# Optimization experiments

Measured on AMD Instinct MI355X. Metric: run time of the kernel, lower is better.

## Reference

```python
import jax, jax.numpy as jnp
import numpy as np

K = 32
TEMPERATURE = 0.1
RTOL, ATOL = 1e-5, 1e-5


def _embed(x, W1, b1, W2, b2, W3, b3):
    h = jax.nn.gelu(x @ W1.T + b1, approximate=False)
    h = jax.nn.gelu(h @ W2.T + b2, approximate=False)
    return jax.nn.sigmoid(h @ W3.T + b3)


def setup_inputs() -> dict:
    key = jax.random.key(0)
    ks = jax.random.split(key, 9)
    Q, N, D_IN, D_E = 256, 16384, 256, 64
    s = lambda fan_in: 1.0 / np.sqrt(fan_in)
    return {
        "x": jax.random.normal(ks[0], (Q, D_IN), jnp.float32),
        "support_x": jax.random.normal(ks[1], (N, D_IN), jnp.float32),
        "support_labels": jax.random.uniform(ks[2], (N, 1), jnp.float32),
        "W1": jax.random.normal(ks[3], (D_E, D_IN), jnp.float32) * s(D_IN),
        "b1": jax.random.normal(ks[4], (D_E,), jnp.float32) * s(D_IN),
        "W2": jax.random.normal(ks[5], (D_E, D_E), jnp.float32) * s(D_E),
        "b2": jax.random.normal(ks[6], (D_E,), jnp.float32) * s(D_E),
        "W3": jax.random.normal(ks[7], (D_E, D_E), jnp.float32) * s(D_E),
        "b3": jax.random.normal(ks[8], (D_E,), jnp.float32) * s(D_E),
    }


def reference(x, support_x, support_labels, W1, b1, W2, b2, W3, b3):
    # query embeddings [Q, D]; support embeddings [N, D] (set_support is no_grad)
    q = _embed(x, W1, b1, W2, b2, W3, b3)
    s = jax.lax.stop_gradient(_embed(support_x, W1, b1, W2, b2, W3, b3))
    # torch.cdist p=2 via expanded squared distances
    d2 = (jnp.sum(q * q, -1)[:, None] + jnp.sum(s * s, -1)[None, :]
          - 2.0 * (q @ s.T))
    dist = jnp.sqrt(jnp.maximum(d2, 0.0))  # [Q, N]
    # isclose mask: |q - s| <= atol + rtol*|s|, all over feature dim
    close = jnp.abs(q[:, None, :] - s[None, :, :]) <= (ATOL + RTOL * jnp.abs(s)[None, :, :])
    mask = jnp.all(close, axis=-1)  # [Q, N]
    dist = jnp.where(mask, jnp.inf, dist)
    # top-k smallest distances
    neg_top, idx = jax.lax.top_k(-dist, K)  # [Q, K]
    topd = -neg_top
    neighbor_labels = support_labels[idx].squeeze(-1)  # [Q, K]
    weights = jax.nn.softmax(-topd / TEMPERATURE, axis=1)
    return jnp.sum(weights * neighbor_labels, axis=1)  # [Q]
```

## Files before the change

kernel.cpp:

```cpp
#include <hip/hip_runtime.h>
#include <math.h>

#define D_IN   256
#define D_E    64
#define N_SUP  16384
#define NQ     256
#define KSEL   32
#define RTOLC  1e-5f
#define ATOLC  1e-5f
#define INV_T  10.0f

#define CHUNK  1024
#define NCH    16
#define QG     8
#define NQG    32

typedef unsigned long long ull;

__device__ __forceinline__ float gelu_exact(float x) {
    return 0.5f * x * (1.0f + erff(x * 0.70710678118654752440f));
}

__global__ __launch_bounds__(256) void prep_w(
    const float* __restrict__ W1, const float* __restrict__ W2,
    const float* __restrict__ W3,
    float* __restrict__ W1T, float* __restrict__ W2T, float* __restrict__ W3T)
{
    const int t = blockIdx.x * 256 + threadIdx.x;
    const int stride = gridDim.x * 256;
    for (int o = t; o < D_E * D_IN; o += stride) {
        int f = o >> 8, k = o & 255;
        W1T[k * D_E + f] = W1[o];
    }
    for (int o = t; o < D_E * D_E; o += stride) {
        int f = o >> 6, k = o & 63;
        W2T[k * D_E + f] = W2[o];
        W3T[k * D_E + f] = W3[o];
    }
}

__global__ __launch_bounds__(512, 6) void embed_kernel(
    const float* __restrict__ sx, const float* __restrict__ x,
    const float* __restrict__ W1T, const float* __restrict__ b1,
    const float* __restrict__ W2T, const float* __restrict__ b2,
    const float* __restrict__ W3T, const float* __restrict__ b3,
    float* __restrict__ s_emb, float* __restrict__ s_norm,
    float* __restrict__ q_emb, float* __restrict__ q_norm)
{
    __shared__ float xc[64][65];
    __shared__ float hA[64][65];
    __shared__ float hB[64][65];
    __shared__ float nsum[64][9];

    const int tid  = threadIdx.x;
    const int lane = tid & 63;
    const int wv   = tid >> 6;
    const int f0   = __builtin_amdgcn_readfirstlane(wv * 8);
    const bool isq = blockIdx.x >= (N_SUP / 64);
    const float* src = isq ? (x + (size_t)(blockIdx.x - N_SUP / 64) * 64 * D_IN)
                           : (sx + (size_t)blockIdx.x * 64 * D_IN);

    float acc[8];
    #pragma unroll
    for (int i = 0; i < 8; ++i) acc[i] = b1[f0 + i];

    for (int kc = 0; kc < 4; ++kc) {
        __syncthreads();
        #pragma unroll
        for (int i = 0; i < 2; ++i) {
            int g   = i * 512 + tid;
            int row = g >> 4;
            int c4  = g & 15;
            float4 v = *reinterpret_cast<const float4*>(
                src + (size_t)row * D_IN + kc * 64 + c4 * 4);
            xc[c4 * 4 + 0][row] = v.x; xc[c4 * 4 + 1][row] = v.y;
            xc[c4 * 4 + 2][row] = v.z; xc[c4 * 4 + 3][row] = v.w;
        }
        __syncthreads();
        const float* wbase = W1T + (size_t)(kc * 64) * D_E + f0;
        #pragma unroll 8
        for (int k = 0; k < 64; ++k) {
            float xk = xc[k][lane];
            const float* wk = wbase + k * D_E;
            #pragma unroll
            for (int f = 0; f < 8; ++f) acc[f] = fmaf(wk[f], xk, acc[f]);
        }
    }
    #pragma unroll
    for (int i = 0; i < 8; ++i) hA[f0 + i][lane] = gelu_exact(acc[i]);
    __syncthreads();

    float a2[8];
    #pragma unroll
    for (int i = 0; i < 8; ++i) a2[i] = b2[f0 + i];
    #pragma unroll 8
    for (int k = 0; k < D_E; ++k) {
        float hk = hA[k][lane];
        const float* wk = W2T + k * D_E + f0;
        #pragma unroll
        for (int f = 0; f < 8; ++f) a2[f] = fmaf(wk[f], hk, a2[f]);
    }
    #pragma unroll
    for (int i = 0; i < 8; ++i) hB[f0 + i][lane] = gelu_exact(a2[i]);
    __syncthreads();

    float a3[8];
    #pragma unroll
    for (int i = 0; i < 8; ++i) a3[i] = b3[f0 + i];
    #pragma unroll 8
    for (int k = 0; k < D_E; ++k) {
        float hk = hB[k][lane];
        const float* wk = W3T + k * D_E + f0;
        #pragma unroll
        for (int f = 0; f < 8; ++f) a3[f] = fmaf(wk[f], hk, a3[f]);
    }
    float e[8];
    float np = 0.0f;
    #pragma unroll
    for (int i = 0; i < 8; ++i) {
        e[i] = 1.0f / (1.0f + expf(-a3[i]));
        np = fmaf(e[i], e[i], np);
    }

    const int rowl = isq ? (blockIdx.x - N_SUP / 64) * 64 + lane
                         : blockIdx.x * 64 + lane;
    float* E   = isq ? q_emb  : s_emb;
    float* Nrm = isq ? q_norm : s_norm;
    float* erow = E + (size_t)rowl * D_E + f0;
    *reinterpret_cast<float4*>(erow)     = make_float4(e[0], e[1], e[2], e[3]);
    *reinterpret_cast<float4*>(erow + 4) = make_float4(e[4], e[5], e[6], e[7]);

    nsum[lane][wv] = np;
    __syncthreads();
    if (wv == 0) {
        float s = 0.0f;
        #pragma unroll
        for (int w = 0; w < 8; ++w) s += nsum[lane][w];
        Nrm[rowl] = s;
    }
}

__global__ __launch_bounds__(512, 4) void knn_phaseA(
    const float* __restrict__ s_emb, const float* __restrict__ s_norm,
    const float* __restrict__ q_emb, const float* __restrict__ q_norm,
    const float* __restrict__ labels, ull* __restrict__ cand)
{
    __shared__ float tile[64 * 68];
    __shared__ float d2l[QG][CHUNK];
    __shared__ ull   win_l[QG][KSEL];

    const int tid  = threadIdx.x;
    const int lane = tid & 63;
    const int wid  = tid >> 6;
    const int qg   = blockIdx.x >> 4;
    const int sc   = blockIdx.x & 15;
    const int qiu  = __builtin_amdgcn_readfirstlane(qg * QG + wid);

    const float* q0 = q_emb + (size_t)qiu * D_E;
    const float  qn = q_norm[qiu];

    for (int s = 0; s < 16; ++s) {
        __syncthreads();
        #pragma unroll
        for (int i = 0; i < 2; ++i) {
            int g   = i * 512 + tid;
            int row = g >> 4, c4 = g & 15;
            float4 v = *reinterpret_cast<const float4*>(
                s_emb + (size_t)(sc * CHUNK + s * 64 + row) * D_E + c4 * 4);
            *reinterpret_cast<float4*>(&tile[row * 68 + c4 * 4]) = v;
        }
        __syncthreads();

        const float* tr = &tile[lane * 68];
        float a = 0.0f;
        #pragma unroll
        for (int c = 0; c < 16; ++c) {
            float4 sv = *reinterpret_cast<const float4*>(tr + c * 4);
            a = fmaf(q0[c * 4 + 0], sv.x, a);
            a = fmaf(q0[c * 4 + 1], sv.y, a);
            a = fmaf(q0[c * 4 + 2], sv.z, a);
            a = fmaf(q0[c * 4 + 3], sv.w, a);
        }
        const int grow = sc * CHUNK + s * 64 + lane;
        float d2 = fmaxf(qn + s_norm[grow] - 2.0f * a, 0.0f);
        if (d2 < 1e-3f) {
            bool close = true;
            for (int k = 0; k < D_E; ++k) {
                float sv = tr[k];
                close = close && (fabsf(q0[k] - sv) <= (ATOLC + RTOLC * fabsf(sv)));
            }
            if (close) d2 = INFINITY;
        }
        d2l[wid][s * 64 + lane] = d2;
    }

    ull sk[16];
    #pragma unroll
    for (int j = 0; j < 16; ++j) {
        float d2 = d2l[wid][j * 64 + lane];
        sk[j] = ((ull)__float_as_uint(d2) << 10) | (unsigned)(j * 64 + lane);
    }

    #pragma unroll
    for (int k = 2; k <= 16; k <<= 1) {
        #pragma unroll
        for (int j = k >> 1; j > 0; j >>= 1) {
            #pragma unroll
            for (int i = 0; i < 16; ++i) {
                int ixj = i ^ j;
                if (ixj > i) {
                    if ((i & k) == 0) {
                        ull a_ = sk[i], b_ = sk[ixj];
                        bool c_ = b_ < a_;
                        sk[i] = c_ ? b_ : a_; sk[ixj] = c_ ? a_ : b_;
                    } else {
                        ull a_ = sk[i], b_ = sk[ixj];
                        bool c_ = a_ < b_;
                        sk[i] = c_ ? b_ : a_; sk[ixj] = c_ ? a_ : b_;
                    }
                }
            }
        }
    }

    ull lkey = sk[0];
    for (int it = 0; it < KSEL; ++it) {
        ull m = lkey;
        #pragma unroll
        for (int off = 1; off < 64; off <<= 1) {
            ull o = __shfl_xor(m, off);
            m = o < m ? o : m;
        }
        if (lane == it) win_l[wid][it] = m;
        if (lkey == m) {
            #pragma unroll
            for (int j = 0; j < 15; ++j) sk[j] = sk[j + 1];
            sk[15] = ~0ull;
            lkey = sk[0];
        }
    }

    if (lane < KSEL) {
        ull m = win_l[wid][lane];
        unsigned gidx = (unsigned)(sc * CHUNK) + (unsigned)(m & 1023u);
        float lab = labels[gidx];
        ull* dst = cand + ((size_t)qiu * NCH + sc) * KSEL;
        dst[lane] = ((ull)(unsigned)(m >> 10) << 32) | (ull)__float_as_uint(lab);
    }
}

__global__ __launch_bounds__(256) void knn_phaseB(
    const ull* __restrict__ cand, float* __restrict__ out)
{
    const int lane = threadIdx.x & 63;
    const int wid  = threadIdx.x >> 6;
    const int q    = blockIdx.x * 4 + wid;

    const bool act = lane < NCH;
    const ull* lst = cand + ((size_t)q * NCH + (lane & 15)) * KSEL;
    int ptr = 0;
    ull cur = act ? lst[0] : ~0ull;

    float d0 = 0.0f, sw = 0.0f, sl = 0.0f;
    for (int it = 0; it < KSEL; ++it) {
        unsigned mv = (unsigned)(cur >> 32);
        unsigned ml = (unsigned)cur;
        #pragma unroll
        for (int off = 1; off < 16; off <<= 1) {
            unsigned ov = __shfl_xor(mv, off);
            unsigned ol = __shfl_xor(ml, off);
            bool take = (ov < mv) || (ov == mv && (lane & off));
            mv = take ? ov : mv;
            ml = take ? ol : ml;
        }
        ull b = __ballot(act && (unsigned)(cur >> 32) == mv);
        int wl = (int)(__ffsll((long long)b) - 1);
        if (lane == wl) {
            ++ptr;
            cur = (ptr < KSEL) ? lst[ptr] : ~0ull;
        }
        if (lane == 0) {
            float d = sqrtf(__uint_as_float(mv));
            if (it == 0) d0 = d;
            float w = expf((d0 - d) * INV_T);
            sw += w;
            sl += w * __uint_as_float(ml);
        }
    }
    if (lane == 0) out[q] = sl / sw;
}

extern "C" void kernel_launch(void* const* d_in, const int* in_sizes, int n_in,
                              void* d_out, int out_size, void* d_ws, size_t ws_size,
                              hipStream_t stream) {
    const float* x      = (const float*)d_in[0];
    const float* sx     = (const float*)d_in[1];
    const float* labels = (const float*)d_in[2];
    const float* W1     = (const float*)d_in[3];
    const float* b1     = (const float*)d_in[4];
    const float* W2     = (const float*)d_in[5];
    const float* b2     = (const float*)d_in[6];
    const float* W3     = (const float*)d_in[7];
    const float* b3     = (const float*)d_in[8];
    float* out = (float*)d_out;

    float* ws     = (float*)d_ws;
    float* s_emb  = ws;
    float* s_norm = s_emb + N_SUP * D_E;
    float* q_emb  = s_norm + N_SUP;
    float* q_norm = q_emb + NQ * D_E;
    float* W1T    = q_norm + NQ;
    float* W2T    = W1T + D_IN * D_E;
    float* W3T    = W2T + D_E * D_E;
    ull*   cand   = (ull*)(W3T + D_E * D_E);

    prep_w<<<32, 256, 0, stream>>>(W1, W2, W3, W1T, W2T, W3T);
    embed_kernel<<<(N_SUP + NQ) / 64, 512, 0, stream>>>(
        sx, x, W1T, b1, W2T, b2, W3T, b3, s_emb, s_norm, q_emb, q_norm);
    knn_phaseA<<<NQG * NCH, 512, 0, stream>>>(s_emb, s_norm, q_emb, q_norm,
                                              labels, cand);
    knn_phaseB<<<NQ / 4, 256, 0, stream>>>(cand, out);
}
```

Measured before the change: 101.6 us.

## Stage MLP weights in shared memory and remap kNN distance lanes

Drops the separate weight-transpose kernel. The embed kernel now loads each weight matrix from global memory and transposes it into a shared buffer, then reads it with vectorized LDS loads instead of scalar global/scalar-cache loads. The hA/hB buffers are reused so shared memory stays about the same. In phaseA each wave now handles 8 queries over 8 tile rows, with the query vectors held in registers. This replaces the earlier pattern of one query per wave reading q from memory per FMA. The cost is 64 extra VGPRs for the query registers and padded d2l rows, plus an added barrier before the sort.

```diff
diff --git a/kernel.cpp b/kernel.cpp
--- a/kernel.cpp
+++ b/kernel.cpp
@@ -21,35 +21,17 @@
     return 0.5f * x * (1.0f + erff(x * 0.70710678118654752440f));
 }
 
-__global__ __launch_bounds__(256) void prep_w(
-    const float* __restrict__ W1, const float* __restrict__ W2,
-    const float* __restrict__ W3,
-    float* __restrict__ W1T, float* __restrict__ W2T, float* __restrict__ W3T)
-{
-    const int t = blockIdx.x * 256 + threadIdx.x;
-    const int stride = gridDim.x * 256;
-    for (int o = t; o < D_E * D_IN; o += stride) {
-        int f = o >> 8, k = o & 255;
-        W1T[k * D_E + f] = W1[o];
-    }
-    for (int o = t; o < D_E * D_E; o += stride) {
-        int f = o >> 6, k = o & 63;
-        W2T[k * D_E + f] = W2[o];
-        W3T[k * D_E + f] = W3[o];
-    }
-}
-
 __global__ __launch_bounds__(512, 6) void embed_kernel(
     const float* __restrict__ sx, const float* __restrict__ x,
-    const float* __restrict__ W1T, const float* __restrict__ b1,
-    const float* __restrict__ W2T, const float* __restrict__ b2,
-    const float* __restrict__ W3T, const float* __restrict__ b3,
+    const float* __restrict__ W1, const float* __restrict__ b1,
+    const float* __restrict__ W2, const float* __restrict__ b2,
+    const float* __restrict__ W3, const float* __restrict__ b3,
     float* __restrict__ s_emb, float* __restrict__ s_norm,
     float* __restrict__ q_emb, float* __restrict__ q_norm)
 {
-    __shared__ float xc[64][65];
+    __shared__ float xcB[64][65];
     __shared__ float hA[64][65];
-    __shared__ float hB[64][65];
+    __shared__ float BW[64 * 68];
     __shared__ float nsum[64][9];
 
     const int tid  = threadIdx.x;
@@ -73,46 +55,88 @@
             int c4  = g & 15;
             float4 v = *reinterpret_cast<const float4*>(
                 src + (size_t)row * D_IN + kc * 64 + c4 * 4);
-            xc[c4 * 4 + 0][row] = v.x; xc[c4 * 4 + 1][row] = v.y;
-            xc[c4 * 4 + 2][row] = v.z; xc[c4 * 4 + 3][row] = v.w;
+            xcB[c4 * 4 + 0][row] = v.x; xcB[c4 * 4 + 1][row] = v.y;
+            xcB[c4 * 4 + 2][row] = v.z; xcB[c4 * 4 + 3][row] = v.w;
+        }
+        #pragma unroll
+        for (int i = 0; i < 2; ++i) {
+            int f  = (tid >> 4) + 32 * i;
+            int c4 = tid & 15;
+            float4 w = *reinterpret_cast<const float4*>(
+                W1 + (size_t)f * D_IN + kc * 64 + c4 * 4);
+            BW[(c4 * 4 + 0) * 68 + f] = w.x; BW[(c4 * 4 + 1) * 68 + f] = w.y;
+            BW[(c4 * 4 + 2) * 68 + f] = w.z; BW[(c4 * 4 + 3) * 68 + f] = w.w;
         }
         __syncthreads();
-        const float* wbase = W1T + (size_t)(kc * 64) * D_E + f0;
         #pragma unroll 8
         for (int k = 0; k < 64; ++k) {
-            float xk = xc[k][lane];
-            const float* wk = wbase + k * D_E;
-            #pragma unroll
-            for (int f = 0; f < 8; ++f) acc[f] = fmaf(wk[f], xk, acc[f]);
-        }
-    }
+            float xk = xcB[k][lane];
+            const float* wk = &BW[k * 68 + f0];
+            float4 w0 = *reinterpret_cast<const float4*>(wk);
+            float4 w1 = *reinterpret_cast<const float4*>(wk + 4);
+            acc[0] = fmaf(w0.x, xk, acc[0]); acc[1] = fmaf(w0.y, xk, acc[1]);
+            acc[2] = fmaf(w0.z, xk, acc[2]); acc[3] = fmaf(w0.w, xk, acc[3]);
+            acc[4] = fmaf(w1.x, xk, acc[4]); acc[5] = fmaf(w1.y, xk, acc[5]);
+            acc[6] = fmaf(w1.z, xk, acc[6]); acc[7] = fmaf(w1.w, xk, acc[7]);
+        }
+    }
+    __syncthreads();
     #pragma unroll
     for (int i = 0; i < 8; ++i) hA[f0 + i][lane] = gelu_exact(acc[i]);
-    __syncthreads();
-
+
+    {
+        #pragma unroll
+        for (int i = 0; i < 2; ++i) {
+            int f  = (tid >> 4) + 32 * i;
+            int c4 = tid & 15;
+            float4 w = *reinterpret_cast<const float4*>(W2 + (size_t)f * D_E + c4 * 4);
+            BW[(c4 * 4 + 0) * 68 + f] = w.x; BW[(c4 * 4 + 1) * 68 + f] = w.y;
+            BW[(c4 * 4 + 2) * 68 + f] = w.z; BW[(c4 * 4 + 3) * 68 + f] = w.w;
+        }
+    }
+    __syncthreads();
     float a2[8];
     #pragma unroll
     for (int i = 0; i < 8; ++i) a2[i] = b2[f0 + i];
     #pragma unroll 8
     for (int k = 0; k < D_E; ++k) {
         float hk = hA[k][lane];
-        const float* wk = W2T + k * D_E + f0;
-        #pragma unroll
-        for (int f = 0; f < 8; ++f) a2[f] = fmaf(wk[f], hk, a2[f]);
-    }
-    #pragma unroll
-    for (int i = 0; i < 8; ++i) hB[f0 + i][lane] = gelu_exact(a2[i]);
-    __syncthreads();
-
+        const float* wk = &BW[k * 68 + f0];
+        float4 w0 = *reinterpret_cast<const float4*>(wk);
+        float4 w1 = *reinterpret_cast<const float4*>(wk + 4);
+        a2[0] = fmaf(w0.x, hk, a2[0]); a2[1] = fmaf(w0.y, hk, a2[1]);
+        a2[2] = fmaf(w0.z, hk, a2[2]); a2[3] = fmaf(w0.w, hk, a2[3]);
+        a2[4] = fmaf(w1.x, hk, a2[4]); a2[5] = fmaf(w1.y, hk, a2[5]);
+        a2[6] = fmaf(w1.z, hk, a2[6]); a2[7] = fmaf(w1.w, hk, a2[7]);
+    }
+    __syncthreads();
+    #pragma unroll
+    for (int i = 0; i < 8; ++i) xcB[f0 + i][lane] = gelu_exact(a2[i]);
+
+    {
+        #pragma unroll
+        for (int i = 0; i < 2; ++i) {
+            int f  = (tid >> 4) + 32 * i;
+            int c4 = tid & 15;
+            float4 w = *reinterpret_cast<const float4*>(W3 + (size_t)f * D_E + c4 * 4);
+            BW[(c4 * 4 + 0) * 68 + f] = w.x; BW[(c4 * 4 + 1) * 68 + f] = w.y;
+            BW[(c4 * 4 + 2) * 68 + f] = w.z; BW[(c4 * 4 + 3) * 68 + f] = w.w;
+        }
+    }
+    __syncthreads();
     float a3[8];
     #pragma unroll
     for (int i = 0; i < 8; ++i) a3[i] = b3[f0 + i];
     #pragma unroll 8
     for (int k = 0; k < D_E; ++k) {
-        float hk = hB[k][lane];
-        const float* wk = W3T + k * D_E + f0;
-        #pragma unroll
-        for (int f = 0; f < 8; ++f) a3[f] = fmaf(wk[f], hk, a3[f]);
+        float hk = xcB[k][lane];
+        const float* wk = &BW[k * 68 + f0];
+        float4 w0 = *reinterpret_cast<const float4*>(wk);
+        float4 w1 = *reinterpret_cast<const float4*>(wk + 4);
+        a3[0] = fmaf(w0.x, hk, a3[0]); a3[1] = fmaf(w0.y, hk, a3[1]);
+        a3[2] = fmaf(w0.z, hk, a3[2]); a3[3] = fmaf(w0.w, hk, a3[3]);
+        a3[4] = fmaf(w1.x, hk, a3[4]); a3[5] = fmaf(w1.y, hk, a3[5]);
+        a3[6] = fmaf(w1.z, hk, a3[6]); a3[7] = fmaf(w1.w, hk, a3[7]);
     }
     float e[8];
     float np = 0.0f;
@@ -146,7 +170,7 @@
     const float* __restrict__ labels, ull* __restrict__ cand)
 {
     __shared__ float tile[64 * 68];
-    __shared__ float d2l[QG][CHUNK];
+    __shared__ float d2l[QG][1032];
     __shared__ ull   win_l[QG][KSEL];
 
     const int tid  = threadIdx.x;
@@ -154,10 +178,15 @@
     const int wid  = tid >> 6;
     const int qg   = blockIdx.x >> 4;
     const int sc   = blockIdx.x & 15;
-    const int qiu  = __builtin_amdgcn_readfirstlane(qg * QG + wid);
-
-    const float* q0 = q_emb + (size_t)qiu * D_E;
-    const float  qn = q_norm[qiu];
+
+    const int  ql   = lane >> 3;
+    const int  rsub = lane & 7;
+    const float* qrow = q_emb + (size_t)(qg * QG + ql) * D_E;
+    float4 qv[16];
+    #pragma unroll
+    for (int c = 0; c < 16; ++c)
+        qv[c] = *reinterpret_cast<const float4*>(qrow + c * 4);
+    const float qn = q_norm[qg * QG + ql];
 
     for (int s = 0; s < 16; ++s) {
         __syncthreads();
@@ -171,28 +200,32 @@
         }
         __syncthreads();
 
-        const float* tr = &tile[lane * 68];
+        const int rloc = wid * 8 + rsub;
+        const float* tr = &tile[rloc * 68];
         float a = 0.0f;
         #pragma unroll
         for (int c = 0; c < 16; ++c) {
             float4 sv = *reinterpret_cast<const float4*>(tr + c * 4);
-            a = fmaf(q0[c * 4 + 0], sv.x, a);
-            a = fmaf(q0[c * 4 + 1], sv.y, a);
-            a = fmaf(q0[c * 4 + 2], sv.z, a);
-            a = fmaf(q0[c * 4 + 3], sv.w, a);
-        }
-        const int grow = sc * CHUNK + s * 64 + lane;
+            a = fmaf(qv[c].x, sv.x, a);
+            a = fmaf(qv[c].y, sv.y, a);
+            a = fmaf(qv[c].z, sv.z, a);
+            a = fmaf(qv[c].w, sv.w, a);
+        }
+        const int grow = sc * CHUNK + s * 64 + rloc;
         float d2 = fmaxf(qn + s_norm[grow] - 2.0f * a, 0.0f);
         if (d2 < 1e-3f) {
             bool close = true;
+            #pragma unroll 8
             for (int k = 0; k < D_E; ++k) {
-                float sv = tr[k];
-                close = close && (fabsf(q0[k] - sv) <= (ATOLC + RTOLC * fabsf(sv)));
+                float svk = tr[k];
+                float qk  = reinterpret_cast<const float*>(qv)[k];
+                close = close && (fabsf(qk - svk) <= (ATOLC + RTOLC * fabsf(svk)));
             }
             if (close) d2 = INFINITY;
         }
-        d2l[wid][s * 64 + lane] = d2;
-    }
+        d2l[ql][s * 64 + rloc] = d2;
+    }
+    __syncthreads();
 
     ull sk[16];
     #pragma unroll
@@ -244,7 +277,7 @@
         ull m = win_l[wid][lane];
         unsigned gidx = (unsigned)(sc * CHUNK) + (unsigned)(m & 1023u);
         float lab = labels[gidx];
-        ull* dst = cand + ((size_t)qiu * NCH + sc) * KSEL;
+        ull* dst = cand + ((size_t)(qg * QG + wid) * NCH + sc) * KSEL;
         dst[lane] = ((ull)(unsigned)(m >> 10) << 32) | (ull)__float_as_uint(lab);
     }
 }
@@ -309,14 +342,10 @@
     float* s_norm = s_emb + N_SUP * D_E;
     float* q_emb  = s_norm + N_SUP;
     float* q_norm = q_emb + NQ * D_E;
-    float* W1T    = q_norm + NQ;
-    float* W2T    = W1T + D_IN * D_E;
-    float* W3T    = W2T + D_E * D_E;
-    ull*   cand   = (ull*)(W3T + D_E * D_E);
-
-    prep_w<<<32, 256, 0, stream>>>(W1, W2, W3, W1T, W2T, W3T);
+    ull*   cand   = (ull*)(q_norm + NQ);
+
     embed_kernel<<<(N_SUP + NQ) / 64, 512, 0, stream>>>(
-        sx, x, W1T, b1, W2T, b2, W3T, b3, s_emb, s_norm, q_emb, q_norm);
+        sx, x, W1, b1, W2, b2, W3, b3, s_emb, s_norm, q_emb, q_norm);
     knn_phaseA<<<NQG * NCH, 512, 0, stream>>>(s_emb, s_norm, q_emb, q_norm,
                                               labels, cand);
     knn_phaseB<<<NQ / 4, 256, 0, stream>>>(cand, out);
```

Measured after the change: 223.7 us. +120.2%, slower.

## Double-buffer embed input staging and remap kNN distance work across queries

Applied to the files above, without the earlier changes.

The embed kernel now double-buffers the input tile in shared memory. Loading chunk kc+1 overlaps the FMA loop on chunk kc, which removes one barrier per chunk, and the hB buffer is folded into xc. Its launch bound drops to 2 blocks per SM to allow more registers. In phaseA each wave now computes distances for 8 queries × 8 support rows with query vectors held in registers instead of one query per wave, adding a barrier before sorting and padding d2l to reduce bank conflicts. This risks register pressure from the 16 float4 query registers and LDS bank conflicts on tile row reads.

```diff
diff --git a/kernel.cpp b/kernel.cpp
--- a/kernel.cpp
+++ b/kernel.cpp
@@ -39,7 +39,7 @@
     }
 }
 
-__global__ __launch_bounds__(512, 6) void embed_kernel(
+__global__ __launch_bounds__(512, 2) void embed_kernel(
     const float* __restrict__ sx, const float* __restrict__ x,
     const float* __restrict__ W1T, const float* __restrict__ b1,
     const float* __restrict__ W2T, const float* __restrict__ b2,
@@ -47,9 +47,8 @@
     float* __restrict__ s_emb, float* __restrict__ s_norm,
     float* __restrict__ q_emb, float* __restrict__ q_norm)
 {
-    __shared__ float xc[64][65];
+    __shared__ float xc[2][64][65];
     __shared__ float hA[64][65];
-    __shared__ float hB[64][65];
     __shared__ float nsum[64][9];
 
     const int tid  = threadIdx.x;
@@ -60,31 +59,45 @@
     const float* src = isq ? (x + (size_t)(blockIdx.x - N_SUP / 64) * 64 * D_IN)
                            : (sx + (size_t)blockIdx.x * 64 * D_IN);
 
+    #define STAGE_X(kc_, buf_)                                                  \
+        {                                                                       \
+            _Pragma("unroll")                                                   \
+            for (int i = 0; i < 2; ++i) {                                       \
+                int g   = i * 512 + tid;                                        \
+                int row = g >> 4, c4 = g & 15;                                  \
+                float4 v = *reinterpret_cast<const float4*>(                    \
+                    src + (size_t)row * D_IN + (kc_) * 64 + c4 * 4);            \
+                xc[buf_][c4 * 4 + 0][row] = v.x;                                \
+                xc[buf_][c4 * 4 + 1][row] = v.y;                                \
+                xc[buf_][c4 * 4 + 2][row] = v.z;                                \
+                xc[buf_][c4 * 4 + 3][row] = v.w;                                \
+            }                                                                   \
+        }
+
+    STAGE_X(0, 0);
+    __syncthreads();
+
     float acc[8];
     #pragma unroll
     for (int i = 0; i < 8; ++i) acc[i] = b1[f0 + i];
 
     for (int kc = 0; kc < 4; ++kc) {
+        if (kc < 3) STAGE_X(kc + 1, (kc + 1) & 1);
+        const int buf = kc & 1;
+        const float* wbase = W1T + (size_t)(kc * 64) * D_E + f0;
+        #pragma unroll
+        for (int k8 = 0; k8 < 64; k8 += 8) {
+            float xk[8];
+            #pragma unroll
+            for (int j = 0; j < 8; ++j) xk[j] = xc[buf][k8 + j][lane];
+            #pragma unroll
+            for (int j = 0; j < 8; ++j) {
+                const float* wk = wbase + (k8 + j) * D_E;
+                #pragma unroll
+                for (int f = 0; f < 8; ++f) acc[f] = fmaf(wk[f], xk[j], acc[f]);
+            }
+        }
         __syncthreads();
-        #pragma unroll
-        for (int i = 0; i < 2; ++i) {
-            int g   = i * 512 + tid;
-            int row = g >> 4;
-            int c4  = g & 15;
-            float4 v = *reinterpret_cast<const float4*>(
-                src + (size_t)row * D_IN + kc * 64 + c4 * 4);
-            xc[c4 * 4 + 0][row] = v.x; xc[c4 * 4 + 1][row] = v.y;
-            xc[c4 * 4 + 2][row] = v.z; xc[c4 * 4 + 3][row] = v.w;
-        }
-        __syncthreads();
-        const float* wbase = W1T + (size_t)(kc * 64) * D_E + f0;
-        #pragma unroll 8
-        for (int k = 0; k < 64; ++k) {
-            float xk = xc[k][lane];
-            const float* wk = wbase + k * D_E;
-            #pragma unroll
-            for (int f = 0; f < 8; ++f) acc[f] = fmaf(wk[f], xk, acc[f]);
-        }
     }
     #pragma unroll
     for (int i = 0; i < 8; ++i) hA[f0 + i][lane] = gelu_exact(acc[i]);
@@ -93,26 +106,36 @@
     float a2[8];
     #pragma unroll
     for (int i = 0; i < 8; ++i) a2[i] = b2[f0 + i];
-    #pragma unroll 8
-    for (int k = 0; k < D_E; ++k) {
-        float hk = hA[k][lane];
-        const float* wk = W2T + k * D_E + f0;
-        #pragma unroll
-        for (int f = 0; f < 8; ++f) a2[f] = fmaf(wk[f], hk, a2[f]);
-    }
-    #pragma unroll
-    for (int i = 0; i < 8; ++i) hB[f0 + i][lane] = gelu_exact(a2[i]);
+    #pragma unroll
+    for (int k8 = 0; k8 < 64; k8 += 8) {
+        float xk[8];
+        #pragma unroll
+        for (int j = 0; j < 8; ++j) xk[j] = hA[k8 + j][lane];
+        #pragma unroll
+        for (int j = 0; j < 8; ++j) {
+            const float* wk = W2T + (k8 + j) * D_E + f0;
+            #pragma unroll
+            for (int f = 0; f < 8; ++f) a2[f] = fmaf(wk[f], xk[j], a2[f]);
+        }
+    }
+    #pragma unroll
+    for (int i = 0; i < 8; ++i) xc[0][f0 + i][lane] = gelu_exact(a2[i]);
     __syncthreads();
 
     float a3[8];
     #pragma unroll
     for (int i = 0; i < 8; ++i) a3[i] = b3[f0 + i];
-    #pragma unroll 8
-    for (int k = 0; k < D_E; ++k) {
-        float hk = hB[k][lane];
-        const float* wk = W3T + k * D_E + f0;
-        #pragma unroll
-        for (int f = 0; f < 8; ++f) a3[f] = fmaf(wk[f], hk, a3[f]);
+    #pragma unroll
+    for (int k8 = 0; k8 < 64; k8 += 8) {
+        float xk[8];
+        #pragma unroll
+        for (int j = 0; j < 8; ++j) xk[j] = xc[0][k8 + j][lane];
+        #pragma unroll
+        for (int j = 0; j < 8; ++j) {
+            const float* wk = W3T + (k8 + j) * D_E + f0;
+            #pragma unroll
+            for (int f = 0; f < 8; ++f) a3[f] = fmaf(wk[f], xk[j], a3[f]);
+        }
     }
     float e[8];
     float np = 0.0f;
@@ -138,6 +161,7 @@
         for (int w = 0; w < 8; ++w) s += nsum[lane][w];
         Nrm[rowl] = s;
     }
+    #undef STAGE_X
 }
 
 __global__ __launch_bounds__(512, 4) void knn_phaseA(
@@ -146,7 +170,7 @@
     const float* __restrict__ labels, ull* __restrict__ cand)
 {
     __shared__ float tile[64 * 68];
-    __shared__ float d2l[QG][CHUNK];
+    __shared__ float d2l[QG][1032];
     __shared__ ull   win_l[QG][KSEL];
 
     const int tid  = threadIdx.x;
@@ -154,10 +178,15 @@
     const int wid  = tid >> 6;
     const int qg   = blockIdx.x >> 4;
     const int sc   = blockIdx.x & 15;
-    const int qiu  = __builtin_amdgcn_readfirstlane(qg * QG + wid);
-
-    const float* q0 = q_emb + (size_t)qiu * D_E;
-    const float  qn = q_norm[qiu];
+
+    const int  ql   = lane >> 3;
+    const int  rsub = lane & 7;
+    const float* qrow = q_emb + (size_t)(qg * QG + ql) * D_E;
+    float4 qv[16];
+    #pragma unroll
+    for (int c = 0; c < 16; ++c)
+        qv[c] = *reinterpret_cast<const float4*>(qrow + c * 4);
+    const float qn = q_norm[qg * QG + ql];
 
     for (int s = 0; s < 16; ++s) {
         __syncthreads();
@@ -171,28 +200,30 @@
         }
         __syncthreads();
 
-        const float* tr = &tile[lane * 68];
+        const int rloc = wid * 8 + rsub;
+        const float* tr = &tile[rloc * 68];
         float a = 0.0f;
         #pragma unroll
         for (int c = 0; c < 16; ++c) {
             float4 sv = *reinterpret_cast<const float4*>(tr + c * 4);
-            a = fmaf(q0[c * 4 + 0], sv.x, a);
-            a = fmaf(q0[c * 4 + 1], sv.y, a);
-            a = fmaf(q0[c * 4 + 2], sv.z, a);
-            a = fmaf(q0[c * 4 + 3], sv.w, a);
-        }
-        const int grow = sc * CHUNK + s * 64 + lane;
+            a = fmaf(qv[c].x, sv.x, a);
+            a = fmaf(qv[c].y, sv.y, a);
+            a = fmaf(qv[c].z, sv.z, a);
+            a = fmaf(qv[c].w, sv.w, a);
+        }
+        const int grow = sc * CHUNK + s * 64 + rloc;
         float d2 = fmaxf(qn + s_norm[grow] - 2.0f * a, 0.0f);
         if (d2 < 1e-3f) {
             bool close = true;
             for (int k = 0; k < D_E; ++k) {
-                float sv = tr[k];
-                close = close && (fabsf(q0[k] - sv) <= (ATOLC + RTOLC * fabsf(sv)));
+                float svk = tr[k];
+                close = close && (fabsf(qrow[k] - svk) <= (ATOLC + RTOLC * fabsf(svk)));
             }
             if (close) d2 = INFINITY;
         }
-        d2l[wid][s * 64 + lane] = d2;
-    }
+        d2l[ql][s * 64 + rloc] = d2;
+    }
+    __syncthreads();
 
     ull sk[16];
     #pragma unroll
@@ -244,7 +275,7 @@
         ull m = win_l[wid][lane];
         unsigned gidx = (unsigned)(sc * CHUNK) + (unsigned)(m & 1023u);
         float lab = labels[gidx];
-        ull* dst = cand + ((size_t)qiu * NCH + sc) * KSEL;
+        ull* dst = cand + ((size_t)(qg * QG + wid) * NCH + sc) * KSEL;
         dst[lane] = ((ull)(unsigned)(m >> 10) << 32) | (ull)__float_as_uint(lab);
     }
 }
```

Measured after the change: 152.1 us. 1.5x slower.
